# Optimization experiments

Measured on AMD Instinct MI355X. Metric: run time of the kernel, lower is better.

The kernel has to match this reference:

```python
import jax, jax.numpy as jnp
import numpy as np

ANCHOR_SIZES = (128.0, 256.0, 512.0)
ASPECT_RATIOS = (0.5, 1.0, 2.0)
NMS_THR = 0.7
KEEP_PRE = 1000    # test_keep_pre_nms
KEEP_POST = 300    # test_keep_post_nms


def make_anchors(fh, fw, img_h, img_w):
    # base anchors per (ratio, size), centered at origin, xyxy
    sizes = jnp.array(ANCHOR_SIZES, jnp.float32)
    ratios = jnp.array(ASPECT_RATIOS, jnp.float32)
    h_r = jnp.sqrt(ratios)
    w_r = 1.0 / h_r
    ws = (w_r[:, None] * sizes[None, :]).reshape(-1)  # [nA]
    hs = (h_r[:, None] * sizes[None, :]).reshape(-1)
    base = jnp.stack([-ws, -hs, ws, hs], axis=1) / 2.0  # [nA,4]
    stride_h = img_h / fh
    stride_w = img_w / fw
    sx = jnp.arange(fw, dtype=jnp.float32) * stride_w
    sy = jnp.arange(fh, dtype=jnp.float32) * stride_h
    yy, xx = jnp.meshgrid(sy, sx, indexing='ij')
    shifts = jnp.stack([xx, yy, xx, yy], axis=-1).reshape(-1, 1, 4)  # [fh*fw,1,4]
    return (shifts + base[None]).reshape(-1, 4)  # [fh*fw*nA,4]


def offsets2boxes(deltas, anchors):
    # deltas: [bs,N,4] (dx,dy,dw,dh); anchors: [N,4] xyxy
    aw = anchors[:, 2] - anchors[:, 0]
    ah = anchors[:, 3] - anchors[:, 1]
    acx = anchors[:, 0] + 0.5 * aw
    acy = anchors[:, 1] + 0.5 * ah
    pcx = deltas[..., 0] * aw + acx
    pcy = deltas[..., 1] * ah + acy
    pw = jnp.exp(deltas[..., 2]) * aw
    ph = jnp.exp(deltas[..., 3]) * ah
    return jnp.stack([pcx - 0.5 * pw, pcy - 0.5 * ph,
                      pcx + 0.5 * pw, pcy + 0.5 * ph], axis=-1)


def nms_single(boxes, scores):
    # boxes [K,4] already sorted by descending score; sequential greedy NMS
    K = boxes.shape[0]
    b = jax.lax.stop_gradient(boxes)
    area = (b[:, 2] - b[:, 0]) * (b[:, 3] - b[:, 1])
    lt = jnp.maximum(b[:, None, :2], b[None, :, :2])
    rb = jnp.minimum(b[:, None, 2:], b[None, :, 2:])
    wh = jnp.clip(rb - lt, 0.0)
    inter = wh[..., 0] * wh[..., 1]
    iou = inter / (area[:, None] + area[None, :] - inter + 1e-9)  # [K,K]
    idx = jnp.arange(K)

    def body(i, keep):
        suppress = (iou[i] > NMS_THR) & keep[i] & (idx > i)
        return keep & ~suppress

    keep = jax.lax.fori_loop(0, K, body, jnp.ones((K,), bool))
    # stable: kept boxes first, preserving score order; pad to KEEP_POST
    order = jnp.argsort((~keep).astype(jnp.int32))[:KEEP_POST]
    valid = keep[order].astype(boxes.dtype)
    dets = jnp.concatenate([boxes[order], scores[order, None]], axis=-1)
    return dets * valid[:, None]  # padded rows are zeros


def setup_inputs() -> dict:
    key = jax.random.key(0)
    ks = jax.random.split(key, 4)
    C = 512
    nA = 9
    return {
        'fmaps': jax.random.normal(ks[0], (8, C, 64, 64), jnp.float32),
        'base_w': jax.random.normal(ks[1], (C, C, 3, 3), jnp.float32) * 0.01,
        'base_b': jnp.zeros((C,), jnp.float32),
        'cls_w': jax.random.normal(ks[2], (nA, C), jnp.float32) * 0.01,
        'cls_b': jnp.zeros((nA,), jnp.float32),
        'reg_w': jax.random.normal(ks[3], (nA * 4, C), jnp.float32) * 0.01,
        'reg_b': jnp.zeros((nA * 4,), jnp.float32),
        'img_h': 1024,
        'img_w': 1024,
    }


def reference(fmaps, base_w, base_b, cls_w, cls_b, reg_w, reg_b, img_h, img_w):
    bs, C, fh, fw = fmaps.shape
    nA = len(ANCHOR_SIZES) * len(ASPECT_RATIOS)
    # PredictionLayer: 3x3 conv + relu, then 1x1 cls / reg convs
    x = jax.lax.conv_general_dilated(
        fmaps, base_w, window_strides=(1, 1), padding='SAME',
        dimension_numbers=('NCHW', 'OIHW', 'NCHW'))
    x = jax.nn.relu(x + base_b[None, :, None, None])
    cls = jnp.einsum('bchw,ac->bahw', x, cls_w) + cls_b[None, :, None, None]
    reg = jnp.einsum('bchw,ac->bahw', x, reg_w) + reg_b[None, :, None, None]
    # flatten_preds: view(bs,nA,c,h,w) -> permute(0,3,4,1,2) -> (bs, h*w*nA, c)
    cls_logits = cls.reshape(bs, nA, 1, fh, fw).transpose(0, 3, 4, 1, 2).reshape(bs, -1, 1)
    reg_deltas = reg.reshape(bs, nA, 4, fh, fw).transpose(0, 3, 4, 1, 2).reshape(bs, -1, 4)
    # DetectionLayer
    anchors = make_anchors(fh, fw, float(img_h), float(img_w))
    scores = jax.nn.sigmoid(cls_logits[..., 0])          # [bs, N]
    boxes = offsets2boxes(reg_deltas, anchors)           # [bs, N, 4]
    _, sel = jax.lax.top_k(scores, KEEP_PRE)             # per-image top-k
    s = jnp.take_along_axis(scores, sel, axis=1)
    b = jnp.take_along_axis(boxes, sel[..., None], axis=1)
    # clip boxes to image
    b = jnp.stack([jnp.clip(b[..., 0], 0.0, float(img_w)),
                   jnp.clip(b[..., 1], 0.0, float(img_h)),
                   jnp.clip(b[..., 2], 0.0, float(img_w)),
                   jnp.clip(b[..., 3], 0.0, float(img_h))], axis=-1)
    # per-image NMS; output padded to fixed [bs, KEEP_POST, 5]
    return jax.vmap(nms_single)(b, s)
```

## Files before the change

### kernel.cpp

```cpp
#include <hip/hip_runtime.h>
#include <math.h>


typedef double f64x4 __attribute__((ext_vector_type(4)));
typedef double f64x2 __attribute__((ext_vector_type(2)));

#define BS 8
#define CIN 512
#define COUT 512
#define FH 64
#define FW 64
#define NA 9
#define NPIX (FH*FW)
#define NANCH (NPIX*NA)
#define NPAD 65536
#define KPRE 1000
#define KPOST 300

#define OFF_X      0ull
#define OFF_SCORES (OFF_X + 134217728ull)
#define OFF_BOXES  (OFF_SCORES + 2359296ull)
#define OFF_KEYS   (OFF_BOXES + 9437184ull)
#define OFF_BUF1   (OFF_KEYS + 4194304ull)
#define OFF_BUF2   (OFF_BUF1 + 1048576ull)
#define OFF_SEL    (OFF_BUF2 + 262144ull)
#define OFF_KEEP   (OFF_SEL + 32768ull)
#define WS_NEEDED  (OFF_KEEP + 32768ull)
#define OFF_MASK   OFF_X
#define WOFF_U        WS_NEEDED
#define WOFF_V        (WOFF_U + 33554432ull)
#define WS_WINO_FULL  (WOFF_V + 67108864ull + 67108864ull)
#define WS_WINO_HALF  (WOFF_V + 33554432ull + 33554432ull)

#define SW_STRIDE 80
#define SW_WORDS  (36 * SW_STRIDE)
#define SI_RSTRIDE 80
#define SI_CSTRIDE 320
#define BUF_WORDS (SW_WORDS + 4 * SI_CSTRIDE)

__device__ __forceinline__ void conv_compute(
    const float* __restrict__ sWp, const float* __restrict__ sIp,
    const int* __restrict__ boff, f64x4 acc[2][4]) {
#pragma unroll
  for (int k0s = 0; k0s < 9; ++k0s) {
    double a0 = (double)sWp[k0s * 4 * SW_STRIDE];
    double a1 = (double)sWp[k0s * 4 * SW_STRIDE + 16];
    const float* bp = sIp + boff[k0s];
    double b0 = (double)bp[0];
    double b1 = (double)bp[16];
    double b2 = (double)bp[32];
    double b3 = (double)bp[48];
    acc[0][0] = __builtin_amdgcn_mfma_f64_16x16x4f64(a0, b0, acc[0][0], 0, 0, 0);
    acc[0][1] = __builtin_amdgcn_mfma_f64_16x16x4f64(a0, b1, acc[0][1], 0, 0, 0);
    acc[0][2] = __builtin_amdgcn_mfma_f64_16x16x4f64(a0, b2, acc[0][2], 0, 0, 0);
    acc[0][3] = __builtin_amdgcn_mfma_f64_16x16x4f64(a0, b3, acc[0][3], 0, 0, 0);
    acc[1][0] = __builtin_amdgcn_mfma_f64_16x16x4f64(a1, b0, acc[1][0], 0, 0, 0);
    acc[1][1] = __builtin_amdgcn_mfma_f64_16x16x4f64(a1, b1, acc[1][1], 0, 0, 0);
    acc[1][2] = __builtin_amdgcn_mfma_f64_16x16x4f64(a1, b2, acc[1][2], 0, 0, 0);
    acc[1][3] = __builtin_amdgcn_mfma_f64_16x16x4f64(a1, b3, acc[1][3], 0, 0, 0);
  }
}

__global__ __launch_bounds__(256, 3) void conv_mfma_kernel(
    const float* __restrict__ fm, const float* __restrict__ W,
    const float* __restrict__ bias, double* __restrict__ x) {
  __shared__ float sbuf[2 * BUF_WORDS];
  const int ocb = blockIdx.x, rp = blockIdx.y, b = blockIdx.z;
  const int h0 = rp * 2;
  const int oc0 = ocb * 64;
  const int tid = threadIdx.x;
  const int wid = tid >> 6, l = tid & 63;
  const int q = l >> 4, r16 = l & 15;
  const int wm = wid >> 1, wn = wid & 1;

  const int wo = tid >> 2, wseg = tid & 3;
  const float* wbase = W + (size_t)(oc0 + wo) * 4608 + wseg * 9;
  const int wlds0 = (wseg * 9) * SW_STRIDE + wo;

  const float* fmb = fm + (size_t)b * CIN * NPIX;
  int ioff[5];
  int idls[5];
  bool sact[5], lact[5];
#pragma unroll
  for (int s = 0; s < 5; ++s) {
    int li = tid + 256 * s;
    sact[s] = li < 1056;
    int li_c = sact[s] ? li : 0;
    int c = li_c / 264, rem = li_c % 264, r = rem / 66, col = rem % 66;
    int gy = h0 - 1 + r, gx = col - 1;
    lact[s] = sact[s] && gy >= 0 && gy < FH && gx >= 0 && gx < FW;
    ioff[s] = lact[s] ? (c * NPIX + gy * FW + gx) : 0;
    idls[s] = SW_WORDS + c * SI_CSTRIDE + r * SI_RSTRIDE + col;
  }

  const int apos = q * SW_STRIDE + wm * 32 + r16;
  const int ipos = SW_WORDS + wn * SI_RSTRIDE + r16;
  int boff[9];
#pragma unroll
  for (int k0s = 0; k0s < 9; ++k0s) {
    int k = k0s * 4 + q;
    int c = k / 9, t = k - 9 * c;
    int dy = t / 3, dx = t - 3 * dy;
    boff[k0s] = c * SI_CSTRIDE + dy * SI_RSTRIDE + dx;
  }

  f64x4 acc[2][4];
#pragma unroll
  for (int tm = 0; tm < 2; ++tm)
#pragma unroll
    for (int tn = 0; tn < 4; ++tn)
#pragma unroll
      for (int v = 0; v < 4; ++v) acc[tm][tn][v] = 0.0;

  float wreg[9], ireg[5];

#define LOAD_REGS(t) do {                                            \
    const int cc_ = 4 * (t);                                         \
    _Pragma("unroll")                                                \
    for (int j = 0; j < 9; ++j) wreg[j] = wbase[cc_ * 9 + j];        \
    _Pragma("unroll")                                                \
    for (int s = 0; s < 5; ++s)                                      \
      ireg[s] = lact[s] ? fmb[(size_t)(ioff[s] + cc_ * NPIX)] : 0.f; \
  } while (0)

#define WRITE_LDS(base) do {                                         \
    _Pragma("unroll")                                                \
    for (int j = 0; j < 9; ++j) (base)[wlds0 + j * SW_STRIDE] = wreg[j]; \
    _Pragma("unroll")                                                \
    for (int s = 0; s < 5; ++s)                                      \
      if (sact[s]) (base)[idls[s]] = ireg[s];                        \
  } while (0)

  float* buf0 = sbuf;
  float* buf1 = sbuf + BUF_WORDS;

  LOAD_REGS(0);
  WRITE_LDS(buf0);
  __syncthreads();

  for (int tt = 0; tt < 64; ++tt) {
    const int t1 = 2 * tt + 1;
    LOAD_REGS(t1);
    __builtin_amdgcn_s_setprio(1);
    conv_compute(buf0 + apos, buf0 + ipos, boff, acc);
    __builtin_amdgcn_s_setprio(0);
    WRITE_LDS(buf1);
    __syncthreads();
    const int t2 = (t1 + 1 < 128) ? t1 + 1 : 127;
    LOAD_REGS(t2);
    __builtin_amdgcn_s_setprio(1);
    conv_compute(buf1 + apos, buf1 + ipos, boff, acc);
    __builtin_amdgcn_s_setprio(0);
    WRITE_LDS(buf0);
    __syncthreads();
  }

  int prow[4], pcol[4];
  {
    f64x4 probe = {0.0, 0.0, 0.0, 0.0};
    double pa = (q == 0) ? (double)r16 : ((q == 1) ? 1.0 : 0.0);
    double pb = (q == 0) ? 1.0 : ((q == 1) ? (double)(16 * r16) : 0.0);
    probe = __builtin_amdgcn_mfma_f64_16x16x4f64(pa, pb, probe, 0, 0, 0);
#pragma unroll
    for (int v = 0; v < 4; ++v) {
      int val = (int)(probe[v] + 0.5);
      prow[v] = val & 15;
      pcol[v] = (val >> 4) & 15;
    }
  }

#pragma unroll
  for (int tm = 0; tm < 2; ++tm) {
#pragma unroll
    for (int v = 0; v < 4; ++v) {
      const int oc = oc0 + wm * 32 + tm * 16 + prow[v];
      const double bv = (double)bias[oc];
      const int h = h0 + wn;
#pragma unroll
      for (int tn = 0; tn < 4; ++tn) {
        const int w = tn * 16 + pcol[v];
        double val = acc[tm][tn][v] + bv;
        val = val > 0.0 ? val : 0.0;
        x[(size_t)(b * COUT + oc) * NPIX + h * FW + w] = val;
      }
    }
  }
#undef LOAD_REGS
#undef WRITE_LDS
}

__global__ __launch_bounds__(256) void wino_wt_kernel(
    const float* __restrict__ W, double* __restrict__ U) {
  const int id = blockIdx.x * 256 + threadIdx.x;
  const int oc = id >> 9, c = id & 511;
  const float* g = W + (size_t)(oc * CIN + c) * 9;
  double g0[3], g1[3], g2[3];
#pragma unroll
  for (int j = 0; j < 3; ++j) {
    g0[j] = (double)g[j];
    g1[j] = (double)g[3 + j];
    g2[j] = (double)g[6 + j];
  }
  double T[4][3];
#pragma unroll
  for (int j = 0; j < 3; ++j) {
    T[0][j] = g0[j];
    T[1][j] = 0.5 * (g0[j] + g1[j] + g2[j]);
    T[2][j] = 0.5 * (g0[j] - g1[j] + g2[j]);
    T[3][j] = g2[j];
  }
  double* Ub = U + (size_t)c * 512 + oc;
#pragma unroll
  for (int xi = 0; xi < 4; ++xi) {
    double u0 = T[xi][0];
    double u1 = 0.5 * (T[xi][0] + T[xi][1] + T[xi][2]);
    double u2 = 0.5 * (T[xi][0] - T[xi][1] + T[xi][2]);
    double u3 = T[xi][2];
    Ub[(size_t)(xi * 4 + 0) * 262144] = u0;
    Ub[(size_t)(xi * 4 + 1) * 262144] = u1;
    Ub[(size_t)(xi * 4 + 2) * 262144] = u2;
    Ub[(size_t)(xi * 4 + 3) * 262144] = u3;
  }
}

template <int T>
__global__ __launch_bounds__(256) void wino_in_kernel(
    const float* __restrict__ fm, double* __restrict__ V, int b, int t0) {
  const int id = blockIdx.x * 256 + threadIdx.x;
  const int c = id / T, rem = id % T;
  const int tyx = t0 + rem;
  const int ty = tyx >> 5, tx = tyx & 31;
  const float* src = fm + (size_t)(b * CIN + c) * NPIX;
  const int y0 = 2 * ty - 1, x0 = 2 * tx - 1;
  double d[4][4];
#pragma unroll
  for (int r = 0; r < 4; ++r) {
    int y = y0 + r;
#pragma unroll
    for (int s = 0; s < 4; ++s) {
      int xx = x0 + s;
      d[r][s] = (y >= 0 && y < FH && xx >= 0 && xx < FW)
                    ? (double)src[y * FW + xx] : 0.0;
    }
  }
  double Z[4][4];
#pragma unroll
  for (int s = 0; s < 4; ++s) {
    Z[0][s] = d[0][s] - d[2][s];
    Z[1][s] = d[1][s] + d[2][s];
    Z[2][s] = d[2][s] - d[1][s];
    Z[3][s] = d[1][s] - d[3][s];
  }
  double* Vb = V + (size_t)c * T + rem;
#pragma unroll
  for (int xi = 0; xi < 4; ++xi) {
    double v0 = Z[xi][0] - Z[xi][2];
    double v1 = Z[xi][1] + Z[xi][2];
    double v2 = Z[xi][2] - Z[xi][1];
    double v3 = Z[xi][1] - Z[xi][3];
    Vb[(size_t)(xi * 4 + 0) * 512 * T] = v0;
    Vb[(size_t)(xi * 4 + 1) * 512 * T] = v1;
    Vb[(size_t)(xi * 4 + 2) * 512 * T] = v2;
    Vb[(size_t)(xi * 4 + 3) * 512 * T] = v3;
  }
}

#define WSU_STRIDE 72
#define WSV_STRIDE 136
#define WSU_WORDS  (8 * WSU_STRIDE)
#define WBUF_WORDS (WSU_WORDS + 8 * WSV_STRIDE)

template <int T>
__global__ __launch_bounds__(256, 3) void wino_gemm_kernel(
    const double* __restrict__ U, const double* __restrict__ V,
    double* __restrict__ M) {
  __shared__ double sbuf[3 * WBUF_WORDS];
  const int tb = blockIdx.x, ocb = blockIdx.y, pos = blockIdx.z;
  const int oc0 = ocb * 64, t0 = tb * 128;
  const int tid = threadIdx.x;
  const int wid = tid >> 6, l = tid & 63;
  const int q = l >> 4, r16 = l & 15;
  const int wm = wid >> 1, wn = wid & 1;

  const int ka = tid >> 5;
  const int oc2 = (tid & 31) * 2;
  const int t4 = (tid & 31) * 4;
  const double* uSrc = U + (size_t)pos * 262144 + (size_t)ka * 512 + oc0 + oc2;
  const double* vSrc = V + (size_t)pos * 512 * T + (size_t)ka * T + t0 + t4;
  const int ua_lds = ka * WSU_STRIDE + oc2;
  const int vb_lds = WSU_WORDS + ka * WSV_STRIDE + t4;

  const int apos = q * WSU_STRIDE + wm * 32 + r16;
  const int bpos = WSU_WORDS + q * WSV_STRIDE + wn * 64 + r16;

  f64x4 acc[2][4];
#pragma unroll
  for (int tm = 0; tm < 2; ++tm)
#pragma unroll
    for (int tn = 0; tn < 4; ++tn)
#pragma unroll
      for (int v = 0; v < 4; ++v) acc[tm][tn][v] = 0.0;

  f64x2 ra, rb0, rb1;
  double fa[2][2], fb[2][4];

#define WLOAD(t) do {                                                  \
    const size_t cc_ = 8 * (size_t)(t);                                \
    ra  = *(const f64x2*)(uSrc + cc_ * 512);                           \
    rb0 = *(const f64x2*)(vSrc + cc_ * T);                             \
    rb1 = *(const f64x2*)(vSrc + cc_ * T + 2);                         \
  } while (0)

#define WSTORE(base) do {                                              \
    (base)[ua_lds] = ra[0]; (base)[ua_lds + 1] = ra[1];                \
    (base)[vb_lds] = rb0[0]; (base)[vb_lds + 1] = rb0[1];              \
    (base)[vb_lds + 2] = rb1[0]; (base)[vb_lds + 3] = rb1[1];          \
  } while (0)

#define FRAGREAD(base) do {                                            \
    _Pragma("unroll")                                                  \
    for (int kg = 0; kg < 2; ++kg) {                                   \
      fa[kg][0] = (base)[apos + kg * 4 * WSU_STRIDE];                  \
      fa[kg][1] = (base)[apos + kg * 4 * WSU_STRIDE + 16];             \
      fb[kg][0] = (base)[bpos + kg * 4 * WSV_STRIDE];                  \
      fb[kg][1] = (base)[bpos + kg * 4 * WSV_STRIDE + 16];             \
      fb[kg][2] = (base)[bpos + kg * 4 * WSV_STRIDE + 32];             \
      fb[kg][3] = (base)[bpos + kg * 4 * WSV_STRIDE + 48];             \
    }                                                                  \
  } while (0)

#define WCOMPUTE() do {                                                \
    _Pragma("unroll")                                                  \
    for (int kg = 0; kg < 2; ++kg) {                                   \
      acc[0][0] = __builtin_amdgcn_mfma_f64_16x16x4f64(fa[kg][0], fb[kg][0], acc[0][0], 0, 0, 0); \
      acc[0][1] = __builtin_amdgcn_mfma_f64_16x16x4f64(fa[kg][0], fb[kg][1], acc[0][1], 0, 0, 0); \
      acc[0][2] = __builtin_amdgcn_mfma_f64_16x16x4f64(fa[kg][0], fb[kg][2], acc[0][2], 0, 0, 0); \
      acc[0][3] = __builtin_amdgcn_mfma_f64_16x16x4f64(fa[kg][0], fb[kg][3], acc[0][3], 0, 0, 0); \
      acc[1][0] = __builtin_amdgcn_mfma_f64_16x16x4f64(fa[kg][1], fb[kg][0], acc[1][0], 0, 0, 0); \
      acc[1][1] = __builtin_amdgcn_mfma_f64_16x16x4f64(fa[kg][1], fb[kg][1], acc[1][1], 0, 0, 0); \
      acc[1][2] = __builtin_amdgcn_mfma_f64_16x16x4f64(fa[kg][1], fb[kg][2], acc[1][2], 0, 0, 0); \
      acc[1][3] = __builtin_amdgcn_mfma_f64_16x16x4f64(fa[kg][1], fb[kg][3], acc[1][3], 0, 0, 0); \
    }                                                                  \
  } while (0)

  double* bA = sbuf;
  double* bB = sbuf + WBUF_WORDS;
  double* bC = sbuf + 2 * WBUF_WORDS;

  WLOAD(0);
  WSTORE(bA);
  WLOAD(1);
  WSTORE(bB);
  __syncthreads();
  FRAGREAD(bA);
  WLOAD(2);

  for (int k = 0; k < 64; ++k) {
    __builtin_amdgcn_s_setprio(1);
    WCOMPUTE();
    __builtin_amdgcn_s_setprio(0);
    FRAGREAD(bB);
    WSTORE(bC);
    const int t3 = (k + 3 < 64) ? k + 3 : 63;
    WLOAD(t3);
    __syncthreads();
    double* tmp = bA; bA = bB; bB = bC; bC = tmp;
  }

  int prow[4], pcol[4];
  {
    f64x4 probe = {0.0, 0.0, 0.0, 0.0};
    double pa = (q == 0) ? (double)r16 : ((q == 1) ? 1.0 : 0.0);
    double pb = (q == 0) ? 1.0 : ((q == 1) ? (double)(16 * r16) : 0.0);
    probe = __builtin_amdgcn_mfma_f64_16x16x4f64(pa, pb, probe, 0, 0, 0);
#pragma unroll
    for (int v = 0; v < 4; ++v) {
      int val = (int)(probe[v] + 0.5);
      prow[v] = val & 15;
      pcol[v] = (val >> 4) & 15;
    }
  }

#pragma unroll
  for (int tm = 0; tm < 2; ++tm) {
#pragma unroll
    for (int v = 0; v < 4; ++v) {
      const int oc = oc0 + wm * 32 + tm * 16 + prow[v];
#pragma unroll
      for (int tn = 0; tn < 4; ++tn) {
        const int col = wn * 64 + tn * 16 + pcol[v];
        M[(size_t)pos * 512 * T + (size_t)oc * T + t0 + col] = acc[tm][tn][v];
      }
    }
  }
#undef WLOAD
#undef WSTORE
#undef FRAGREAD
#undef WCOMPUTE
}

template <int T>
__global__ __launch_bounds__(256) void wino_out_kernel(
    const double* __restrict__ M, const float* __restrict__ bias,
    double* __restrict__ x, int b, int t0) {
  const int id = blockIdx.x * 256 + threadIdx.x;
  const int oc = id / T, rem = id % T;
  const int tyx = t0 + rem;
  const int ty = tyx >> 5, tx = tyx & 31;
  double m[4][4];
#pragma unroll
  for (int xi = 0; xi < 4; ++xi)
#pragma unroll
    for (int nu = 0; nu < 4; ++nu)
      m[xi][nu] = M[(size_t)(xi * 4 + nu) * 512 * T + (size_t)oc * T + rem];
  double P[2][4];
#pragma unroll
  for (int nu = 0; nu < 4; ++nu) {
    P[0][nu] = m[0][nu] + m[1][nu] + m[2][nu];
    P[1][nu] = m[1][nu] - m[2][nu] - m[3][nu];
  }
  const double bv = (double)bias[oc];
  double* xb = x + (size_t)(b * COUT + oc) * NPIX + (2 * ty) * FW + 2 * tx;
#pragma unroll
  for (int i = 0; i < 2; ++i) {
    double y0 = P[i][0] + P[i][1] + P[i][2] + bv;
    double y1 = P[i][1] - P[i][2] - P[i][3] + bv;
    y0 = y0 > 0.0 ? y0 : 0.0;
    y1 = y1 > 0.0 ? y1 : 0.0;
    xb[i * FW] = y0;
    xb[i * FW + 1] = y1;
  }
}

#define HX_STRIDE 72
#define HW_STRIDE 52
#define HSX_WORDS (16 * HX_STRIDE)
#define HBUF_WORDS (HSX_WORDS + 16 * HW_STRIDE)

__device__ __forceinline__ void heads_compute(
    const double* __restrict__ sA, const double* __restrict__ sB,
    f64x4 acc[3]) {
#pragma unroll
  for (int k0s = 0; k0s < 4; ++k0s) {
    double a0 = sA[k0s * 4 * HW_STRIDE];
    double a1 = sA[k0s * 4 * HW_STRIDE + 16];
    double a2 = sA[k0s * 4 * HW_STRIDE + 32];
    double b0 = sB[k0s * 4 * HX_STRIDE];
    acc[0] = __builtin_amdgcn_mfma_f64_16x16x4f64(a0, b0, acc[0], 0, 0, 0);
    acc[1] = __builtin_amdgcn_mfma_f64_16x16x4f64(a1, b0, acc[1], 0, 0, 0);
    acc[2] = __builtin_amdgcn_mfma_f64_16x16x4f64(a2, b0, acc[2], 0, 0, 0);
  }
}

__global__ __launch_bounds__(256) void heads_mfma_kernel(
    const double* __restrict__ x, const float* __restrict__ cls_w,
    const float* __restrict__ cls_b, const float* __restrict__ reg_w,
    const float* __restrict__ reg_b, const int* __restrict__ img_h,
    const int* __restrict__ img_w, double* __restrict__ scores,
    double* __restrict__ boxes, unsigned long long* __restrict__ keys) {
  __shared__ double sh[2 * HBUF_WORDS];
  const int pxb = blockIdx.x, b = blockIdx.y;
  const int tid = threadIdx.x;
  const int wid = tid >> 6, l = tid & 63;
  const int q = l >> 4, r16 = l & 15;
  const int wn = wid;

  const double* xbase = x + (size_t)b * CIN * NPIX + pxb * 64;
  int sxk[4], sxp[4];
#pragma unroll
  for (int s = 0; s < 4; ++s) {
    int i = tid + 256 * s;
    sxk[s] = i >> 6; sxp[s] = i & 63;
  }
  int swk[3], swo[3];
#pragma unroll
  for (int s = 0; s < 3; ++s) {
    int i = tid + 256 * s;
    swk[s] = i / 48; swo[s] = i % 48;
  }

  const int aposh = HSX_WORDS + q * HW_STRIDE + r16;
  const int bposh = q * HX_STRIDE + wn * 16 + r16;

  f64x4 acc[3];
#pragma unroll
  for (int mt = 0; mt < 3; ++mt)
#pragma unroll
    for (int v = 0; v < 4; ++v) acc[mt][v] = 0.0;

  double xr[4], wr[3];

#define HLOAD(t) do {                                                    \
    const int cc_ = 16 * (t);                                            \
    _Pragma("unroll")                                                    \
    for (int s = 0; s < 4; ++s)                                          \
      xr[s] = xbase[(size_t)(cc_ + sxk[s]) * NPIX + sxp[s]];             \
    _Pragma("unroll")                                                    \
    for (int s = 0; s < 3; ++s) {                                        \
      int o = swo[s], k = cc_ + swk[s];                                  \
      wr[s] = (o < 9) ? (double)cls_w[o * CIN + k]                       \
            : (o < 45) ? (double)reg_w[(o - 9) * CIN + k] : 0.0;         \
    }                                                                    \
  } while (0)

#define HSTORE(base) do {                                                \
    _Pragma("unroll")                                                    \
    for (int s = 0; s < 4; ++s) (base)[sxk[s] * HX_STRIDE + sxp[s]] = xr[s]; \
    _Pragma("unroll")                                                    \
    for (int s = 0; s < 3; ++s)                                          \
      (base)[HSX_WORDS + swk[s] * HW_STRIDE + swo[s]] = wr[s];           \
  } while (0)

  double* buf0 = sh;
  double* buf1 = sh + HBUF_WORDS;

  HLOAD(0);
  HSTORE(buf0);
  __syncthreads();

  for (int tt = 0; tt < 16; ++tt) {
    const int t1 = 2 * tt + 1;
    HLOAD(t1);
    __builtin_amdgcn_s_setprio(1);
    heads_compute(buf0 + aposh, buf0 + bposh, acc);
    __builtin_amdgcn_s_setprio(0);
    HSTORE(buf1);
    __syncthreads();
    const int t2 = (t1 + 1 < 32) ? t1 + 1 : 31;
    HLOAD(t2);
    __builtin_amdgcn_s_setprio(1);
    heads_compute(buf1 + aposh, buf1 + bposh, acc);
    __builtin_amdgcn_s_setprio(0);
    HSTORE(buf0);
    __syncthreads();
  }

  int prow[4], pcol[4];
  {
    f64x4 probe = {0.0, 0.0, 0.0, 0.0};
    double pa = (q == 0) ? (double)r16 : ((q == 1) ? 1.0 : 0.0);
    double pb = (q == 0) ? 1.0 : ((q == 1) ? (double)(16 * r16) : 0.0);
    probe = __builtin_amdgcn_mfma_f64_16x16x4f64(pa, pb, probe, 0, 0, 0);
#pragma unroll
    for (int v = 0; v < 4; ++v) {
      int val = (int)(probe[v] + 0.5);
      prow[v] = val & 15;
      pcol[v] = (val >> 4) & 15;
    }
  }

  double* slog = sh;
#pragma unroll
  for (int mt = 0; mt < 3; ++mt) {
#pragma unroll
    for (int v = 0; v < 4; ++v) {
      const int o = mt * 16 + prow[v];
      if (o < 45) {
        double bv = (o < 9) ? (double)cls_b[o] : (double)reg_b[o - 9];
        slog[o * HX_STRIDE + wn * 16 + pcol[v]] = acc[mt][v] + bv;
      }
    }
  }
  __syncthreads();

  const double ih = (double)img_h[0], iw = (double)img_w[0];
  const double sth = ih / (double)FH, stw = iw / (double)FW;
  const double ratios[3] = {0.5, 1.0, 2.0};
  const double sizes[3] = {128.0, 256.0, 512.0};

  for (int it = tid; it < 576; it += 256) {
    int px = it / 9, a = it % 9;
    int p = pxb * 64 + px;
    int hh = p >> 6, ww = p & 63;
    double z = slog[a * HX_STRIDE + px];
    double score = 1.0 / (1.0 + exp(-z));
    double d0 = slog[(9 + a * 4 + 0) * HX_STRIDE + px];
    double d1 = slog[(9 + a * 4 + 1) * HX_STRIDE + px];
    double d2 = slog[(9 + a * 4 + 2) * HX_STRIDE + px];
    double d3 = slog[(9 + a * 4 + 3) * HX_STRIDE + px];
    double ratio = ratios[a / 3], size = sizes[a % 3];
    double hr = sqrt(ratio), wr_ = 1.0 / hr;
    double wsz = wr_ * size, hsz = hr * size;
    double sxc = (double)ww * stw, syc = (double)hh * sth;
    double ax0 = sxc - wsz * 0.5, ax1 = sxc + wsz * 0.5;
    double ay0 = syc - hsz * 0.5, ay1 = syc + hsz * 0.5;
    double aw = ax1 - ax0, ah = ay1 - ay0;
    double acx = ax0 + 0.5 * aw, acy = ay0 + 0.5 * ah;
    double pcx = d0 * aw + acx, pcy = d1 * ah + acy;
    double pw = exp(d2) * aw, ph = exp(d3) * ah;
    double bx0 = pcx - 0.5 * pw, by0 = pcy - 0.5 * ph;
    double bx1 = pcx + 0.5 * pw, by1 = pcy + 0.5 * ph;
    bx0 = fmin(fmax(bx0, 0.0), iw); bx1 = fmin(fmax(bx1, 0.0), iw);
    by0 = fmin(fmax(by0, 0.0), ih); by1 = fmin(fmax(by1, 0.0), ih);
    long n = (long)p * 9 + a;
    long base = (long)b * NANCH + n;
    boxes[base * 4 + 0] = bx0; boxes[base * 4 + 1] = by0;
    boxes[base * 4 + 2] = bx1; boxes[base * 4 + 3] = by1;
    scores[base] = score;
    unsigned long long bits = (unsigned long long)__double_as_longlong(score);
    keys[(long)b * NPAD + n] =
        ~((bits & 0xFFFFFFFFFFFF0000ull) | (0xFFFFull - (unsigned long long)n));
  }
#undef HLOAD
#undef HSTORE
}

__device__ inline void bitonic4096(unsigned long long* s, int tid) {
  for (int k = 2; k <= 4096; k <<= 1) {
    for (int j = k >> 1; j > 0; j >>= 1) {
#pragma unroll 2
      for (int t = tid; t < 2048; t += 1024) {
        int i = ((t & ~(j - 1)) << 1) | (t & (j - 1));
        int p = i | j;
        bool up = ((i & k) == 0);
        unsigned long long a = s[i], c = s[p];
        if ((a > c) == up) { s[i] = c; s[p] = a; }
      }
      __syncthreads();
    }
  }
}

__global__ __launch_bounds__(1024) void sort_topk_kernel(
    const unsigned long long* __restrict__ in, unsigned long long* __restrict__ out,
    long in_stride, long out_stride) {
  __shared__ unsigned long long s[4096];
  const int b = blockIdx.y, q = blockIdx.x, tid = threadIdx.x;
  const unsigned long long* ip = in + (long)b * in_stride + (long)q * 4096;
#pragma unroll 4
  for (int l = tid; l < 4096; l += 1024) s[l] = ip[l];
  __syncthreads();
  bitonic4096(s, tid);
  unsigned long long* op = out + (long)b * out_stride + (long)q * 1024;
  op[tid] = s[tid];
}

__global__ __launch_bounds__(1024) void sort_final_kernel(
    const unsigned long long* __restrict__ in, int* __restrict__ sel) {
  __shared__ unsigned long long s[4096];
  const int b = blockIdx.x, tid = threadIdx.x;
  const unsigned long long* ip = in + (long)b * 4096;
#pragma unroll 4
  for (int l = tid; l < 4096; l += 1024) s[l] = ip[l];
  __syncthreads();
  bitonic4096(s, tid);
  if (tid < KPRE) sel[b * 1024 + tid] = (int)(s[tid] & 0xFFFFull);
}

__global__ __launch_bounds__(256) void nms_mask_kernel(
    const double* __restrict__ boxes, const int* __restrict__ sel,
    unsigned long long* __restrict__ mask) {
  __shared__ double X0[KPRE], Y0[KPRE], X1[KPRE], Y1[KPRE], AR[KPRE];
  const int ig = blockIdx.x, b = blockIdx.y, tid = threadIdx.x;
  for (int r = tid; r < KPRE; r += 256) {
    int n = sel[b * 1024 + r];
    const double* bp = boxes + ((long)b * NANCH + n) * 4;
    double x0 = bp[0], y0 = bp[1], x1 = bp[2], y1 = bp[3];
    X0[r] = x0; Y0[r] = y0; X1[r] = x1; Y1[r] = y1;
    AR[r] = (x1 - x0) * (y1 - y0);
  }
  __syncthreads();
  const int i = ig * 16 + (tid >> 4);
  const int w = tid & 15;
  if (i >= KPRE) return;
  const double xi0 = X0[i], yi0 = Y0[i], xi1 = X1[i], yi1 = Y1[i], ai = AR[i];
  unsigned long long m = 0;
#pragma unroll 8
  for (int jj = 0; jj < 64; ++jj) {
    int jo = (jj + w) & 63;
    int j = w * 64 + jo;
    if (j < KPRE && j > i) {
      double lx = fmax(xi0, X0[j]), ly = fmax(yi0, Y0[j]);
      double rx = fmin(xi1, X1[j]), ry = fmin(yi1, Y1[j]);
      double ww_ = fmax(rx - lx, 0.0);
      double hh_ = fmax(ry - ly, 0.0);
      double inter = ww_ * hh_;
      double iou = inter / (ai + AR[j] - inter + 1e-9);
      if (iou > 0.7) m |= (1ull << jo);
    }
  }
  mask[((size_t)b * 1024 + i) * 16 + w] = m;
}

__global__ __launch_bounds__(256) void nms_scan_kernel(
    const unsigned long long* __restrict__ mask, int* __restrict__ keep) {
  __shared__ unsigned long long smask[16384];
  __shared__ unsigned long long skeep[16];
  const int b = blockIdx.x, tid = threadIdx.x;
  const unsigned long long* mb = mask + (size_t)b * 1024 * 16;
  for (int l = tid; l < KPRE * 16; l += 256) smask[l] = mb[l];
  __syncthreads();
  if (tid < 64) {
    const int lane16 = tid & 15;
    unsigned long long mykeep = ~0ull;
    unsigned long long p0, p1, p2, p3, p4, p5, p6, p7,
                       p8, p9, p10, p11, p12, p13, p14, p15;
    p0  = smask[0 * 16 + lane16];  p1  = smask[1 * 16 + lane16];
    p2  = smask[2 * 16 + lane16];  p3  = smask[3 * 16 + lane16];
    p4  = smask[4 * 16 + lane16];  p5  = smask[5 * 16 + lane16];
    p6  = smask[6 * 16 + lane16];  p7  = smask[7 * 16 + lane16];
    p8  = smask[8 * 16 + lane16];  p9  = smask[9 * 16 + lane16];
    p10 = smask[10 * 16 + lane16]; p11 = smask[11 * 16 + lane16];
    p12 = smask[12 * 16 + lane16]; p13 = smask[13 * 16 + lane16];
    p14 = smask[14 * 16 + lane16]; p15 = smask[15 * 16 + lane16];
#define NMS_STEP(j) do {                                                   \
      const int ii = i + (j);                                              \
      unsigned long long kw = __shfl(mykeep, ii >> 6);                     \
      bool on = (ii < KPRE) && ((kw >> (ii & 63)) & 1ull);                 \
      mykeep &= ~(on ? p##j : 0ull);                                       \
      p##j = smask[(ii + 16) * 16 + lane16];                               \
    } while (0)
    for (int i = 0; i < 1008; i += 16) {
      NMS_STEP(0);  NMS_STEP(1);  NMS_STEP(2);  NMS_STEP(3);
      NMS_STEP(4);  NMS_STEP(5);  NMS_STEP(6);  NMS_STEP(7);
      NMS_STEP(8);  NMS_STEP(9);  NMS_STEP(10); NMS_STEP(11);
      NMS_STEP(12); NMS_STEP(13); NMS_STEP(14); NMS_STEP(15);
    }
#undef NMS_STEP
    if (tid < 16) skeep[tid] = mykeep;
  }
  __syncthreads();
  for (int r = tid; r < KPRE; r += 256)
    keep[b * 1024 + r] = (int)((skeep[r >> 6] >> (r & 63)) & 1ull);
}

__global__ __launch_bounds__(1024) void out_kernel(
    const double* __restrict__ boxes, const double* __restrict__ scores,
    const int* __restrict__ sel, const int* __restrict__ keep,
    float* __restrict__ out) {
  const int b = blockIdx.x, tid = threadIdx.x;
  int kv = (tid < KPRE) ? keep[b * 1024 + tid] : 0;
  unsigned long long m = __ballot(kv != 0);
  int lane = tid & 63, wid = tid >> 6;
  __shared__ int wcnt[16], woff[16], tot;
  if (lane == 0) wcnt[wid] = __popcll(m);
  __syncthreads();
  if (tid == 0) {
    int s = 0;
    for (int w2 = 0; w2 < 16; ++w2) { woff[w2] = s; s += wcnt[w2]; }
    tot = s;
  }
  __syncthreads();
  int before = __popcll(m & ((1ull << lane) - 1ull));
  int pref = woff[wid] + before;
  if (tid < KPRE) {
    int pos = kv ? pref : (tot + (tid - pref));
    if (pos < KPOST) {
      float* o = out + ((long)b * KPOST + pos) * 5;
      if (kv) {
        int n = sel[b * 1024 + tid];
        const double* bp = boxes + ((long)b * NANCH + n) * 4;
        o[0] = (float)bp[0]; o[1] = (float)bp[1];
        o[2] = (float)bp[2]; o[3] = (float)bp[3];
        o[4] = (float)scores[(long)b * NANCH + n];
      } else {
        o[0] = 0.f; o[1] = 0.f; o[2] = 0.f; o[3] = 0.f; o[4] = 0.f;
      }
    }
  }
}

extern "C" void kernel_launch(void* const* d_in, const int* in_sizes, int n_in,
                              void* d_out, int out_size, void* d_ws, size_t ws_size,
                              hipStream_t stream) {
  const float* fm     = (const float*)d_in[0];
  const float* base_w = (const float*)d_in[1];
  const float* base_b = (const float*)d_in[2];
  const float* cls_w  = (const float*)d_in[3];
  const float* cls_b  = (const float*)d_in[4];
  const float* reg_w  = (const float*)d_in[5];
  const float* reg_b  = (const float*)d_in[6];
  const int* img_h    = (const int*)d_in[7];
  const int* img_w    = (const int*)d_in[8];
  float* out          = (float*)d_out;

  if (ws_size < WS_NEEDED) return;

  char* ws = (char*)d_ws;
  double* x                 = (double*)(ws + OFF_X);
  double* scores            = (double*)(ws + OFF_SCORES);
  double* boxes             = (double*)(ws + OFF_BOXES);
  unsigned long long* keys  = (unsigned long long*)(ws + OFF_KEYS);
  unsigned long long* buf1  = (unsigned long long*)(ws + OFF_BUF1);
  unsigned long long* buf2  = (unsigned long long*)(ws + OFF_BUF2);
  int* sel                  = (int*)(ws + OFF_SEL);
  int* keep                 = (int*)(ws + OFF_KEEP);
  unsigned long long* mask  = (unsigned long long*)(ws + OFF_MASK);

  hipMemsetAsync(ws + OFF_KEYS, 0xFF, 4194304ull + 1048576ull, stream);

  if (ws_size >= WS_WINO_FULL) {
    double* U = (double*)(ws + WOFF_U);
    double* V = (double*)(ws + WOFF_V);
    double* M = (double*)(ws + WOFF_V + 67108864ull);
    wino_wt_kernel<<<dim3(1024), dim3(256), 0, stream>>>(base_w, U);
    for (int b = 0; b < BS; ++b) {
      wino_in_kernel<1024><<<dim3(2048), dim3(256), 0, stream>>>(fm, V, b, 0);
      wino_gemm_kernel<1024><<<dim3(8, 8, 16), dim3(256), 0, stream>>>(U, V, M);
      wino_out_kernel<1024><<<dim3(2048), dim3(256), 0, stream>>>(M, base_b, x, b, 0);
    }
  } else if (ws_size >= WS_WINO_HALF) {
    double* U = (double*)(ws + WOFF_U);
    double* V = (double*)(ws + WOFF_V);
    double* M = (double*)(ws + WOFF_V + 33554432ull);
    wino_wt_kernel<<<dim3(1024), dim3(256), 0, stream>>>(base_w, U);
    for (int b = 0; b < BS; ++b) {
      for (int t0 = 0; t0 < 1024; t0 += 512) {
        wino_in_kernel<512><<<dim3(1024), dim3(256), 0, stream>>>(fm, V, b, t0);
        wino_gemm_kernel<512><<<dim3(4, 8, 16), dim3(256), 0, stream>>>(U, V, M);
        wino_out_kernel<512><<<dim3(1024), dim3(256), 0, stream>>>(M, base_b, x, b, t0);
      }
    }
  } else {
    conv_mfma_kernel<<<dim3(8, 32, 8), dim3(256), 0, stream>>>(fm, base_w, base_b, x);
  }

  heads_mfma_kernel<<<dim3(64, 8), dim3(256), 0, stream>>>(
      x, cls_w, cls_b, reg_w, reg_b, img_h, img_w, scores, boxes, keys);
  sort_topk_kernel<<<dim3(9, 8), dim3(1024), 0, stream>>>(keys, buf1, 65536, 16384);
  sort_topk_kernel<<<dim3(4, 8), dim3(1024), 0, stream>>>(buf1, buf2, 16384, 4096);
  sort_final_kernel<<<dim3(8), dim3(1024), 0, stream>>>(buf2, sel);
  nms_mask_kernel<<<dim3(64, 8), dim3(256), 0, stream>>>(boxes, sel, mask);
  nms_scan_kernel<<<dim3(8), dim3(256), 0, stream>>>(mask, keep);
  out_kernel<<<dim3(8), dim3(1024), 0, stream>>>(boxes, scores, sel, keep, out);
}
```

Measured before the change: 2.029 ms.

## Load Winograd GEMM fragments directly from global memory, dropping LDS staging

The FP64 MFMA Winograd GEMM no longer stages U/V tiles through a triple-buffered shared-memory pipeline with barriers. Each wave now reads its MFMA fragments straight from global memory into registers, using a two-stage register double buffer. This removes LDS traffic and __syncthreads. In exchange, each wave issues scattered 8-byte global loads and re-reads data that waves sharing a tile previously got from LDS, so it relies on the cache and adds latency exposure.

```diff
diff --git a/kernel.cpp b/kernel.cpp
--- a/kernel.cpp
+++ b/kernel.cpp
@@ -265,16 +265,10 @@
   }
 }
 
-#define WSU_STRIDE 72
-#define WSV_STRIDE 136
-#define WSU_WORDS  (8 * WSU_STRIDE)
-#define WBUF_WORDS (WSU_WORDS + 8 * WSV_STRIDE)
-
 template <int T>
 __global__ __launch_bounds__(256, 3) void wino_gemm_kernel(
     const double* __restrict__ U, const double* __restrict__ V,
     double* __restrict__ M) {
-  __shared__ double sbuf[3 * WBUF_WORDS];
   const int tb = blockIdx.x, ocb = blockIdx.y, pos = blockIdx.z;
   const int oc0 = ocb * 64, t0 = tb * 128;
   const int tid = threadIdx.x;
@@ -282,16 +276,10 @@
   const int q = l >> 4, r16 = l & 15;
   const int wm = wid >> 1, wn = wid & 1;
 
-  const int ka = tid >> 5;
-  const int oc2 = (tid & 31) * 2;
-  const int t4 = (tid & 31) * 4;
-  const double* uSrc = U + (size_t)pos * 262144 + (size_t)ka * 512 + oc0 + oc2;
-  const double* vSrc = V + (size_t)pos * 512 * T + (size_t)ka * T + t0 + t4;
-  const int ua_lds = ka * WSU_STRIDE + oc2;
-  const int vb_lds = WSU_WORDS + ka * WSV_STRIDE + t4;
-
-  const int apos = q * WSU_STRIDE + wm * 32 + r16;
-  const int bpos = WSU_WORDS + q * WSV_STRIDE + wn * 64 + r16;
+  const double* uB = U + (size_t)pos * 262144 + (size_t)q * 512
+                     + oc0 + wm * 32 + r16;
+  const double* vB = V + (size_t)pos * 512 * T + (size_t)q * T
+                     + t0 + wn * 64 + r16;
 
   f64x4 acc[2][4];
 #pragma unroll
@@ -301,70 +289,48 @@
 #pragma unroll
       for (int v = 0; v < 4; ++v) acc[tm][tn][v] = 0.0;
 
-  f64x2 ra, rb0, rb1;
   double fa[2][2], fb[2][4];
-
-#define WLOAD(t) do {                                                  \
-    const size_t cc_ = 8 * (size_t)(t);                                \
-    ra  = *(const f64x2*)(uSrc + cc_ * 512);                           \
-    rb0 = *(const f64x2*)(vSrc + cc_ * T);                             \
-    rb1 = *(const f64x2*)(vSrc + cc_ * T + 2);                         \
-  } while (0)
-
-#define WSTORE(base) do {                                              \
-    (base)[ua_lds] = ra[0]; (base)[ua_lds + 1] = ra[1];                \
-    (base)[vb_lds] = rb0[0]; (base)[vb_lds + 1] = rb0[1];              \
-    (base)[vb_lds + 2] = rb1[0]; (base)[vb_lds + 3] = rb1[1];          \
-  } while (0)
-
-#define FRAGREAD(base) do {                                            \
+  double na[2][2], nb[2][4];
+
+#define GLOAD(da, db, t) do {                                          \
     _Pragma("unroll")                                                  \
     for (int kg = 0; kg < 2; ++kg) {                                   \
-      fa[kg][0] = (base)[apos + kg * 4 * WSU_STRIDE];                  \
-      fa[kg][1] = (base)[apos + kg * 4 * WSU_STRIDE + 16];             \
-      fb[kg][0] = (base)[bpos + kg * 4 * WSV_STRIDE];                  \
-      fb[kg][1] = (base)[bpos + kg * 4 * WSV_STRIDE + 16];             \
-      fb[kg][2] = (base)[bpos + kg * 4 * WSV_STRIDE + 32];             \
-      fb[kg][3] = (base)[bpos + kg * 4 * WSV_STRIDE + 48];             \
+      const size_t ro = (size_t)(8 * (t) + 4 * kg);                    \
+      da[kg][0] = uB[ro * 512];                                        \
+      da[kg][1] = uB[ro * 512 + 16];                                   \
+      db[kg][0] = vB[ro * T];                                          \
+      db[kg][1] = vB[ro * T + 16];                                     \
+      db[kg][2] = vB[ro * T + 32];                                     \
+      db[kg][3] = vB[ro * T + 48];                                     \
     }                                                                  \
   } while (0)
 
-#define WCOMPUTE() do {                                                \
+#define WCOMPUTE(da, db) do {                                          \
     _Pragma("unroll")                                                  \
     for (int kg = 0; kg < 2; ++kg) {                                   \
-      acc[0][0] = __builtin_amdgcn_mfma_f64_16x16x4f64(fa[kg][0], fb[kg][0], acc[0][0], 0, 0, 0); \
-      acc[0][1] = __builtin_amdgcn_mfma_f64_16x16x4f64(fa[kg][0], fb[kg][1], acc[0][1], 0, 0, 0); \
-      acc[0][2] = __builtin_amdgcn_mfma_f64_16x16x4f64(fa[kg][0], fb[kg][2], acc[0][2], 0, 0, 0); \
-      acc[0][3] = __builtin_amdgcn_mfma_f64_16x16x4f64(fa[kg][0], fb[kg][3], acc[0][3], 0, 0, 0); \
-      acc[1][0] = __builtin_amdgcn_mfma_f64_16x16x4f64(fa[kg][1], fb[kg][0], acc[1][0], 0, 0, 0); \
-      acc[1][1] = __builtin_amdgcn_mfma_f64_16x16x4f64(fa[kg][1], fb[kg][1], acc[1][1], 0, 0, 0); \
-      acc[1][2] = __builtin_amdgcn_mfma_f64_16x16x4f64(fa[kg][1], fb[kg][2], acc[1][2], 0, 0, 0); \
-      acc[1][3] = __builtin_amdgcn_mfma_f64_16x16x4f64(fa[kg][1], fb[kg][3], acc[1][3], 0, 0, 0); \
+      acc[0][0] = __builtin_amdgcn_mfma_f64_16x16x4f64(da[kg][0], db[kg][0], acc[0][0], 0, 0, 0); \
+      acc[0][1] = __builtin_amdgcn_mfma_f64_16x16x4f64(da[kg][0], db[kg][1], acc[0][1], 0, 0, 0); \
+      acc[0][2] = __builtin_amdgcn_mfma_f64_16x16x4f64(da[kg][0], db[kg][2], acc[0][2], 0, 0, 0); \
+      acc[0][3] = __builtin_amdgcn_mfma_f64_16x16x4f64(da[kg][0], db[kg][3], acc[0][3], 0, 0, 0); \
+      acc[1][0] = __builtin_amdgcn_mfma_f64_16x16x4f64(da[kg][1], db[kg][0], acc[1][0], 0, 0, 0); \
+      acc[1][1] = __builtin_amdgcn_mfma_f64_16x16x4f64(da[kg][1], db[kg][1], acc[1][1], 0, 0, 0); \
+      acc[1][2] = __builtin_amdgcn_mfma_f64_16x16x4f64(da[kg][1], db[kg][2], acc[1][2], 0, 0, 0); \
+      acc[1][3] = __builtin_amdgcn_mfma_f64_16x16x4f64(da[kg][1], db[kg][3], acc[1][3], 0, 0, 0); \
     }                                                                  \
   } while (0)
 
-  double* bA = sbuf;
-  double* bB = sbuf + WBUF_WORDS;
-  double* bC = sbuf + 2 * WBUF_WORDS;
-
-  WLOAD(0);
-  WSTORE(bA);
-  WLOAD(1);
-  WSTORE(bB);
-  __syncthreads();
-  FRAGREAD(bA);
-  WLOAD(2);
-
-  for (int k = 0; k < 64; ++k) {
+  GLOAD(fa, fb, 0);
+  for (int kk = 0; kk < 32; ++kk) {
+    const int k1 = 2 * kk + 1;
+    GLOAD(na, nb, k1);
     __builtin_amdgcn_s_setprio(1);
-    WCOMPUTE();
+    WCOMPUTE(fa, fb);
     __builtin_amdgcn_s_setprio(0);
-    FRAGREAD(bB);
-    WSTORE(bC);
-    const int t3 = (k + 3 < 64) ? k + 3 : 63;
-    WLOAD(t3);
-    __syncthreads();
-    double* tmp = bA; bA = bB; bB = bC; bC = tmp;
+    const int k2 = (k1 + 1 < 64) ? k1 + 1 : 63;
+    GLOAD(fa, fb, k2);
+    __builtin_amdgcn_s_setprio(1);
+    WCOMPUTE(na, nb);
+    __builtin_amdgcn_s_setprio(0);
   }
 
   int prow[4], pcol[4];
@@ -393,9 +359,7 @@
       }
     }
   }
-#undef WLOAD
-#undef WSTORE
-#undef FRAGREAD
+#undef GLOAD
 #undef WCOMPUTE
 }
 
```

Result: faster. 1.745 ms, median of 2 (-14.0%).
